# Optimization experiments

Hardware: AMD Instinct MI355X
Metric: run time of the kernel (lower is better)

## Reference

```python
import jax, jax.numpy as jnp
import numpy as np

D = 1024

def setup_inputs() -> dict:
    key = jax.random.key(0)
    ks = jax.random.split(key, 7)
    s = 1.0 / np.sqrt(D)
    return {
        "x": jax.random.normal(ks[0], (4, 2048, D), dtype=jnp.float32),
        "Wq": jax.random.uniform(ks[1], (D, D), jnp.float32, -s, s),
        "bq": jax.random.uniform(ks[2], (D,), jnp.float32, -s, s),
        "Wk": jax.random.uniform(ks[3], (D, D), jnp.float32, -s, s),
        "bk": jax.random.uniform(ks[4], (D,), jnp.float32, -s, s),
        "Wv": jax.random.uniform(ks[5], (D, D), jnp.float32, -s, s),
        "bv": jax.random.uniform(ks[6], (D,), jnp.float32, -s, s),
    }

def reference(x, Wq, bq, Wk, bk, Wv, bv):
    # x: [b, s, d]; Linear layers: y = x @ W^T + b (torch convention)
    q = jnp.einsum('bsd,ed->bse', x, Wq) + bq
    k = jnp.einsum('bsd,ed->bse', x, Wk) + bk
    v = jnp.einsum('bsd,ed->bse', x, Wv) + bv
    # NOTE: original module does NOT scale by 1/sqrt(d)
    scores = jnp.einsum('bqd,bkd->bqk', q, k)  # [b, s, s]
    attn = jax.nn.softmax(scores, axis=-1)
    return jnp.einsum('bqk,bkd->bqd', attn, v)
```

## Files before the change

kernel.cpp:

```cpp
#include <hip/hip_runtime.h>

typedef _Float16 half8 __attribute__((ext_vector_type(8)));
typedef float floatx4 __attribute__((ext_vector_type(4)));

__device__ __forceinline__ void gld_lds16(const void* g, void* l) {
  __builtin_amdgcn_global_load_lds(
      (const __attribute__((address_space(1))) void*)g,
      (__attribute__((address_space(3))) void*)l, 16, 0, 0);
}

#define SB() __builtin_amdgcn_sched_barrier(0)
#define LGKM(n) asm volatile("s_waitcnt lgkmcnt(" #n ")" ::: "memory")
#define VMC0() asm volatile("s_waitcnt vmcnt(0)" ::: "memory")
#define BAR() __builtin_amdgcn_s_barrier()
#define PRIO1() __builtin_amdgcn_s_setprio(1)
#define PRIO0() __builtin_amdgcn_s_setprio(0)

template <int MODE>
__global__ __launch_bounds__(512, 2) void gemmr(
    const _Float16* __restrict__ Ag, const _Float16* __restrict__ Bg,
    void* __restrict__ Cg, const float* __restrict__ bcat) {
  constexpr int TN   = MODE == 0 ? 192 : (MODE == 1 ? 256 : 128);
  constexpr int KS   = MODE == 0 ? 1024 : (MODE == 1 ? 3072 : 2048);
  constexpr int NK   = MODE == 2 ? 32 : 16;
  constexpr int NWG  = MODE == 0 ? 512 : 256;
  constexpr int WN   = MODE == 1 ? 4 : 2;
  constexpr int NMF  = MODE == 1 ? 8 : 4;
  constexpr int NNF  = TN / 16 / WN;
  constexpr int ASL  = 16384;
  constexpr int BSL  = TN * 64;
  constexpr int NSB  = TN / 64;
  constexpr int CSTR = MODE == 0 ? 3072 : (MODE == 1 ? 2048 : 1024);

  int g = (int)blockIdx.x;
  g = (g & 7) * (NWG / 8) + (g >> 3);

  int row0, col0;
  const _Float16 *Ap, *Bp;
  _Float16* C16 = nullptr;
  float* C32 = nullptr;
  if constexpr (MODE == 0) {
    const int tm = g >> 4, tn = g & 15;
    row0 = tm * 256; col0 = tn * 192;
    Ap = Ag + (size_t)row0 * 1024;
    Bp = Bg + (size_t)col0 * 1024;
    C16 = (_Float16*)Cg;
  } else if constexpr (MODE == 1) {
    const int z = g >> 6, r = g & 63, tm = r >> 3, tn = r & 7;
    row0 = tm * 256; col0 = tn * 256;
    Ap = Ag + (size_t)z * 6291456 + (size_t)row0 * 3072;
    Bp = Ag + (size_t)z * 6291456 + (size_t)col0 * 3072 + 1024;
    C16 = (_Float16*)Cg + (size_t)z * 4194304;
  } else {
    const int z = g >> 6, r = g & 63, tm = r >> 3, tn = r & 7;
    row0 = tm * 256; col0 = tn * 128;
    Ap = Ag + (size_t)z * 4194304 + (size_t)row0 * 2048;
    Bp = Bg + (size_t)z * 2097152 + (size_t)col0 * 2048;
    C32 = (float*)Cg + (size_t)z * 2097152;
  }

  __shared__ _Float16 lds[2 * ASL + 2 * BSL];
  const int tid = threadIdx.x, lane = tid & 63, wid = tid >> 6;
  const int wm = MODE == 1 ? (wid >> 2) : (wid >> 1);
  const int wn = MODE == 1 ? (wid & 3) : (wid & 1);
  const int wrow = wm * (NMF * 16);
  const int wcol = wn * (NNF * 16);
  const int fr = lane & 15, u = lane >> 4, w7 = lane & 7;
  const int k0e = ((u ^ w7) << 3), k1e = (((4 + u) ^ w7) << 3);
  const int srow = tid >> 3;
  const int sgl = (((tid & 7) ^ (srow & 7)) << 3);

  floatx4 acc[NMF][NNF] = {};
  half8 aF[NMF * 2], bF[NNF * 2];

  auto stage1 = [&](const _Float16* Gp, int rowoff, int kt, int dst) {
    gld_lds16(Gp + (size_t)(rowoff + srow) * KS + kt + sgl, &lds[dst + tid * 8]);
  };
  auto stageT = [&](int kt, int p) {
#pragma unroll
    for (int c = 0; c < 4; ++c) stage1(Ap, c * 64, kt, p * ASL + c * 4096);
#pragma unroll
    for (int c = 0; c < NSB; ++c)
      stage1(Bp, c * 64, kt, 2 * ASL + p * BSL + c * 4096);
  };
  auto ldA4 = [&](int p, int mf0) {
#pragma unroll
    for (int mf = 0; mf < 4; ++mf) {
      const int ro = p * ASL + (wrow + (mf0 + mf) * 16 + fr) * 64;
      aF[(mf0 + mf) * 2 + 0] = *(const half8*)&lds[ro + k0e];
      aF[(mf0 + mf) * 2 + 1] = *(const half8*)&lds[ro + k1e];
    }
  };
  auto ldB2 = [&](int p, int nf0) {
#pragma unroll
    for (int nf = 0; nf < 2; ++nf) {
      const int ro = 2 * ASL + p * BSL + (wcol + (nf0 + nf) * 16 + fr) * 64;
      bF[(nf0 + nf) * 2 + 0] = *(const half8*)&lds[ro + k0e];
      bF[(nf0 + nf) * 2 + 1] = *(const half8*)&lds[ro + k1e];
    }
  };
  auto burst = [&](int mf0, int nf0) {
#pragma unroll
    for (int mf = 0; mf < 4; ++mf)
#pragma unroll
      for (int nf = 0; nf < 2; ++nf)
#pragma unroll
        for (int kk = 0; kk < 2; ++kk)
          acc[mf0 + mf][nf0 + nf] = __builtin_amdgcn_mfma_f32_16x16x32_f16(
              aF[(mf0 + mf) * 2 + kk], bF[(nf0 + nf) * 2 + kk],
              acc[mf0 + mf][nf0 + nf], 0, 0, 0);
  };

  stageT(0, 0);
  VMC0();
  BAR();

#pragma unroll 1
  for (int t = 0; t < NK; ++t) {
    const int p = t & 1;
    if (t + 1 < NK) stageT(t * 64 + 64, p ^ 1);
    SB();
    if constexpr (MODE == 1) {
      ldA4(p, 0); SB(); ldB2(p, 0); SB(); ldB2(p, 2); SB(); ldA4(p, 4); SB();
      LGKM(12); SB(); PRIO1(); burst(0, 0); PRIO0(); SB();
      LGKM(8);  SB(); PRIO1(); burst(0, 2); PRIO0(); SB();
      LGKM(0);  SB(); PRIO1(); burst(4, 0); burst(4, 2); PRIO0(); SB();
    } else if constexpr (MODE == 0) {
      ldA4(p, 0); SB(); ldB2(p, 0); SB(); ldB2(p, 2); SB(); ldB2(p, 4); SB();
      LGKM(8); SB(); PRIO1(); burst(0, 0); PRIO0(); SB();
      LGKM(4); SB(); PRIO1(); burst(0, 2); PRIO0(); SB();
      LGKM(0); SB(); PRIO1(); burst(0, 4); PRIO0(); SB();
    } else {
      ldA4(p, 0); SB(); ldB2(p, 0); SB(); ldB2(p, 2); SB();
      LGKM(4); SB(); PRIO1(); burst(0, 0); PRIO0(); SB();
      LGKM(0); SB(); PRIO1(); burst(0, 2); PRIO0(); SB();
    }
    if (t + 1 < NK) VMC0();
    BAR();
  }

  const int r0 = row0 + wrow + u * 4;
  const int c0 = col0 + wcol + fr;
#pragma unroll
  for (int mf = 0; mf < NMF; ++mf)
#pragma unroll
    for (int nf = 0; nf < NNF; ++nf) {
      const int col = c0 + nf * 16;
      float badd = 0.f;
      if constexpr (MODE == 0) badd = bcat[col];
#pragma unroll
      for (int j = 0; j < 4; ++j) {
        const int row = r0 + mf * 16 + j;
        if constexpr (MODE == 2)
          C32[(size_t)row * CSTR + col] = acc[mf][nf][j];
        else
          C16[(size_t)row * CSTR + col] = (_Float16)(acc[mf][nf][j] + badd);
      }
    }
}

__global__ void cvt_f32_f16(const float* __restrict__ in, _Float16* __restrict__ out, int n8) {
  int i = blockIdx.x * blockDim.x + threadIdx.x;
  const int stride = gridDim.x * blockDim.x;
  for (; i < n8; i += stride) {
    const float4* p = (const float4*)(in + (size_t)i * 8);
    float4 a = p[0], b = p[1];
    half8 h;
    h[0] = (_Float16)a.x; h[1] = (_Float16)a.y; h[2] = (_Float16)a.z; h[3] = (_Float16)a.w;
    h[4] = (_Float16)b.x; h[5] = (_Float16)b.y; h[6] = (_Float16)b.z; h[7] = (_Float16)b.w;
    *(half8*)(out + (size_t)i * 8) = h;
  }
}

__global__ void cvt3_w(const float* __restrict__ wq, const float* __restrict__ wk,
                       const float* __restrict__ wv, _Float16* __restrict__ out) {
  const float* in = blockIdx.y == 0 ? wq : (blockIdx.y == 1 ? wk : wv);
  _Float16* o = out + (size_t)blockIdx.y * 1048576;
  const int i = blockIdx.x * blockDim.x + threadIdx.x;
  const float4* p = (const float4*)(in + (size_t)i * 8);
  float4 a = p[0], b = p[1];
  half8 h;
  h[0] = (_Float16)a.x; h[1] = (_Float16)a.y; h[2] = (_Float16)a.z; h[3] = (_Float16)a.w;
  h[4] = (_Float16)b.x; h[5] = (_Float16)b.y; h[6] = (_Float16)b.z; h[7] = (_Float16)b.w;
  *(half8*)(o + (size_t)i * 8) = h;
}

__global__ void bias_cat(const float* __restrict__ a, const float* __restrict__ b,
                         const float* __restrict__ c, float* __restrict__ o) {
  const int i = blockIdx.x * 256 + threadIdx.x;
  const float* s = i < 1024 ? a : (i < 2048 ? b : c);
  o[i] = s[i & 1023];
}

__global__ __launch_bounds__(256) void transpose_v(const _Float16* __restrict__ QKV,
                                                   _Float16* __restrict__ Vt) {
  __shared__ _Float16 t[32][36];
  const int b = blockIdx.z;
  const int e0 = blockIdx.x * 32;
  const int s0 = blockIdx.y * 32;
  const int tid = threadIdx.x;
  const int r = tid >> 3;
  const int c4 = (tid & 7) * 4;
  const _Float16* src = QKV + (size_t)(b * 2048 + s0 + r) * 3072 + 2048 + e0 + c4;
#pragma unroll
  for (int j = 0; j < 4; ++j) t[r][c4 + j] = src[j];
  __syncthreads();
  _Float16* dst = Vt + ((size_t)b * 1024 + e0 + r) * 2048 + s0 + c4;
#pragma unroll
  for (int j = 0; j < 4; ++j) dst[j] = t[c4 + j][r];
}

__global__ __launch_bounds__(256) void softmax_rows_f16(_Float16* __restrict__ S) {
  __shared__ float red[4];
  _Float16* s = S + (size_t)blockIdx.x * 2048;
  const int tid = threadIdx.x;
  float v[8];
  {
    half8 h = *(const half8*)(s + tid * 8);
#pragma unroll
    for (int j = 0; j < 8; ++j) v[j] = (float)h[j];
  }
  float m = v[0];
#pragma unroll
  for (int j = 1; j < 8; ++j) m = fmaxf(m, v[j]);
#pragma unroll
  for (int off = 32; off > 0; off >>= 1) m = fmaxf(m, __shfl_xor(m, off));
  if ((tid & 63) == 0) red[tid >> 6] = m;
  __syncthreads();
  m = fmaxf(fmaxf(red[0], red[1]), fmaxf(red[2], red[3]));
  float sum = 0.f;
#pragma unroll
  for (int j = 0; j < 8; ++j) { v[j] = __expf(v[j] - m); sum += v[j]; }
#pragma unroll
  for (int off = 32; off > 0; off >>= 1) sum += __shfl_xor(sum, off);
  __syncthreads();
  if ((tid & 63) == 0) red[tid >> 6] = sum;
  __syncthreads();
  sum = red[0] + red[1] + red[2] + red[3];
  const float inv = 1.0f / sum;
  half8 h;
#pragma unroll
  for (int j = 0; j < 8; ++j) h[j] = (_Float16)(v[j] * inv);
  *(half8*)(s + tid * 8) = h;
}

extern "C" void kernel_launch(void* const* d_in, const int* in_sizes, int n_in,
                              void* d_out, int out_size, void* d_ws, size_t ws_size,
                              hipStream_t stream) {
  (void)in_sizes; (void)n_in; (void)out_size;
  const float* x  = (const float*)d_in[0];
  const float* Wq = (const float*)d_in[1];
  const float* bq = (const float*)d_in[2];
  const float* Wk = (const float*)d_in[3];
  const float* bk = (const float*)d_in[4];
  const float* Wv = (const float*)d_in[5];
  const float* bv = (const float*)d_in[6];
  float* out = (float*)d_out;

  char* ws = (char*)d_ws;
  size_t off = 0;
  auto alloc = [&](size_t bytes) {
    char* p = ws + off;
    off += (bytes + 255) & ~255ull;
    return p;
  };
  _Float16* x16  = (_Float16*)alloc(8192ull * 1024 * 2);
  _Float16* W16  = (_Float16*)alloc(3072ull * 1024 * 2);
  _Float16* QKV  = (_Float16*)alloc(8192ull * 3072 * 2);
  _Float16* Vt   = (_Float16*)alloc(4096ull * 1024 * 4);
  _Float16* Sc   = (_Float16*)alloc(4ull * 2048 * 2048 * 2);
  float*    bcat = (float*)alloc(3072 * 4);
  if (off > ws_size) return;

  cvt_f32_f16<<<2048, 256, 0, stream>>>(x, x16, 8192 * 1024 / 8);
  cvt3_w<<<dim3(512, 3), 256, 0, stream>>>(Wq, Wk, Wv, W16);
  bias_cat<<<12, 256, 0, stream>>>(bq, bk, bv, bcat);

  gemmr<0><<<512, 512, 0, stream>>>(x16, W16, QKV, bcat);
  transpose_v<<<dim3(32, 64, 4), 256, 0, stream>>>(QKV, Vt);

  gemmr<1><<<256, 512, 0, stream>>>(QKV, QKV, Sc, nullptr);
  softmax_rows_f16<<<8192, 256, 0, stream>>>(Sc);
  gemmr<2><<<256, 512, 0, stream>>>(Sc, Vt, out, nullptr);
}
```

Before: 163.0 us.

## Use uniform 128x128 GEMM tiles with 256 threads and fuse prep kernels

Replaces the large per-mode GEMM tiles (256x192, 256x256, 256x128 with 512 threads) with a single 128x128 tile using 4 waves, which raises the workgroup count for all three GEMMs. The three small conversion/bias kernels are merged into one prep launch to cut launch overhead. Smaller tiles lower per-tile arithmetic intensity and add global/LDS traffic, but they fill the CUs better and use less LDS, so more workgroups can be resident.

After: 158.8 us. 2.5% less time.

```diff
diff --git a/kernel.cpp b/kernel.cpp
--- a/kernel.cpp
+++ b/kernel.cpp
@@ -17,19 +17,12 @@
 #define PRIO0() __builtin_amdgcn_s_setprio(0)
 
 template <int MODE>
-__global__ __launch_bounds__(512, 2) void gemmr(
+__global__ __launch_bounds__(256, 2) void gemmd(
     const _Float16* __restrict__ Ag, const _Float16* __restrict__ Bg,
     void* __restrict__ Cg, const float* __restrict__ bcat) {
-  constexpr int TN   = MODE == 0 ? 192 : (MODE == 1 ? 256 : 128);
   constexpr int KS   = MODE == 0 ? 1024 : (MODE == 1 ? 3072 : 2048);
   constexpr int NK   = MODE == 2 ? 32 : 16;
-  constexpr int NWG  = MODE == 0 ? 512 : 256;
-  constexpr int WN   = MODE == 1 ? 4 : 2;
-  constexpr int NMF  = MODE == 1 ? 8 : 4;
-  constexpr int NNF  = TN / 16 / WN;
-  constexpr int ASL  = 16384;
-  constexpr int BSL  = TN * 64;
-  constexpr int NSB  = TN / 64;
+  constexpr int NWG  = MODE == 0 ? 1536 : (MODE == 1 ? 1024 : 512);
   constexpr int CSTR = MODE == 0 ? 3072 : (MODE == 1 ? 2048 : 1024);
 
   int g = (int)blockIdx.x;
@@ -40,75 +33,71 @@
   _Float16* C16 = nullptr;
   float* C32 = nullptr;
   if constexpr (MODE == 0) {
-    const int tm = g >> 4, tn = g & 15;
-    row0 = tm * 256; col0 = tn * 192;
+    const int tm = g / 24, tn = g % 24;
+    row0 = tm * 128; col0 = tn * 128;
     Ap = Ag + (size_t)row0 * 1024;
     Bp = Bg + (size_t)col0 * 1024;
     C16 = (_Float16*)Cg;
   } else if constexpr (MODE == 1) {
-    const int z = g >> 6, r = g & 63, tm = r >> 3, tn = r & 7;
-    row0 = tm * 256; col0 = tn * 256;
+    const int z = g >> 8, r = g & 255, tm = r >> 4, tn = r & 15;
+    row0 = tm * 128; col0 = tn * 128;
     Ap = Ag + (size_t)z * 6291456 + (size_t)row0 * 3072;
     Bp = Ag + (size_t)z * 6291456 + (size_t)col0 * 3072 + 1024;
     C16 = (_Float16*)Cg + (size_t)z * 4194304;
   } else {
-    const int z = g >> 6, r = g & 63, tm = r >> 3, tn = r & 7;
-    row0 = tm * 256; col0 = tn * 128;
+    const int z = g >> 7, r = g & 127, tm = r >> 3, tn = r & 7;
+    row0 = tm * 128; col0 = tn * 128;
     Ap = Ag + (size_t)z * 4194304 + (size_t)row0 * 2048;
     Bp = Bg + (size_t)z * 2097152 + (size_t)col0 * 2048;
     C32 = (float*)Cg + (size_t)z * 2097152;
   }
 
-  __shared__ _Float16 lds[2 * ASL + 2 * BSL];
+  __shared__ _Float16 lds[32768];
   const int tid = threadIdx.x, lane = tid & 63, wid = tid >> 6;
-  const int wm = MODE == 1 ? (wid >> 2) : (wid >> 1);
-  const int wn = MODE == 1 ? (wid & 3) : (wid & 1);
-  const int wrow = wm * (NMF * 16);
-  const int wcol = wn * (NNF * 16);
+  const int wm = wid >> 1, wn = wid & 1;
+  const int wrow = wm * 64, wcol = wn * 64;
   const int fr = lane & 15, u = lane >> 4, w7 = lane & 7;
   const int k0e = ((u ^ w7) << 3), k1e = (((4 + u) ^ w7) << 3);
   const int srow = tid >> 3;
   const int sgl = (((tid & 7) ^ (srow & 7)) << 3);
 
-  floatx4 acc[NMF][NNF] = {};
-  half8 aF[NMF * 2], bF[NNF * 2];
+  floatx4 acc[4][4] = {};
+  half8 aF[8], bF[8];
 
   auto stage1 = [&](const _Float16* Gp, int rowoff, int kt, int dst) {
     gld_lds16(Gp + (size_t)(rowoff + srow) * KS + kt + sgl, &lds[dst + tid * 8]);
   };
   auto stageT = [&](int kt, int p) {
 #pragma unroll
-    for (int c = 0; c < 4; ++c) stage1(Ap, c * 64, kt, p * ASL + c * 4096);
-#pragma unroll
-    for (int c = 0; c < NSB; ++c)
-      stage1(Bp, c * 64, kt, 2 * ASL + p * BSL + c * 4096);
-  };
-  auto ldA4 = [&](int p, int mf0) {
+    for (int c = 0; c < 4; ++c) stage1(Ap, c * 32, kt, p * 8192 + c * 2048);
+#pragma unroll
+    for (int c = 0; c < 4; ++c) stage1(Bp, c * 32, kt, 16384 + p * 8192 + c * 2048);
+  };
+  auto ldA4 = [&](int p) {
 #pragma unroll
     for (int mf = 0; mf < 4; ++mf) {
-      const int ro = p * ASL + (wrow + (mf0 + mf) * 16 + fr) * 64;
-      aF[(mf0 + mf) * 2 + 0] = *(const half8*)&lds[ro + k0e];
-      aF[(mf0 + mf) * 2 + 1] = *(const half8*)&lds[ro + k1e];
+      const int ro = p * 8192 + (wrow + mf * 16 + fr) * 64;
+      aF[mf * 2 + 0] = *(const half8*)&lds[ro + k0e];
+      aF[mf * 2 + 1] = *(const half8*)&lds[ro + k1e];
     }
   };
   auto ldB2 = [&](int p, int nf0) {
 #pragma unroll
     for (int nf = 0; nf < 2; ++nf) {
-      const int ro = 2 * ASL + p * BSL + (wcol + (nf0 + nf) * 16 + fr) * 64;
+      const int ro = 16384 + p * 8192 + (wcol + (nf0 + nf) * 16 + fr) * 64;
       bF[(nf0 + nf) * 2 + 0] = *(const half8*)&lds[ro + k0e];
       bF[(nf0 + nf) * 2 + 1] = *(const half8*)&lds[ro + k1e];
     }
   };
-  auto burst = [&](int mf0, int nf0) {
+  auto burst = [&](int nf0) {
 #pragma unroll
     for (int mf = 0; mf < 4; ++mf)
 #pragma unroll
       for (int nf = 0; nf < 2; ++nf)
 #pragma unroll
         for (int kk = 0; kk < 2; ++kk)
-          acc[mf0 + mf][nf0 + nf] = __builtin_amdgcn_mfma_f32_16x16x32_f16(
-              aF[(mf0 + mf) * 2 + kk], bF[(nf0 + nf) * 2 + kk],
-              acc[mf0 + mf][nf0 + nf], 0, 0, 0);
+          acc[mf][nf0 + nf] = __builtin_amdgcn_mfma_f32_16x16x32_f16(
+              aF[mf * 2 + kk], bF[(nf0 + nf) * 2 + kk], acc[mf][nf0 + nf], 0, 0, 0);
   };
 
   stageT(0, 0);
@@ -120,21 +109,9 @@
     const int p = t & 1;
     if (t + 1 < NK) stageT(t * 64 + 64, p ^ 1);
     SB();
-    if constexpr (MODE == 1) {
-      ldA4(p, 0); SB(); ldB2(p, 0); SB(); ldB2(p, 2); SB(); ldA4(p, 4); SB();
-      LGKM(12); SB(); PRIO1(); burst(0, 0); PRIO0(); SB();
-      LGKM(8);  SB(); PRIO1(); burst(0, 2); PRIO0(); SB();
-      LGKM(0);  SB(); PRIO1(); burst(4, 0); burst(4, 2); PRIO0(); SB();
-    } else if constexpr (MODE == 0) {
-      ldA4(p, 0); SB(); ldB2(p, 0); SB(); ldB2(p, 2); SB(); ldB2(p, 4); SB();
-      LGKM(8); SB(); PRIO1(); burst(0, 0); PRIO0(); SB();
-      LGKM(4); SB(); PRIO1(); burst(0, 2); PRIO0(); SB();
-      LGKM(0); SB(); PRIO1(); burst(0, 4); PRIO0(); SB();
-    } else {
-      ldA4(p, 0); SB(); ldB2(p, 0); SB(); ldB2(p, 2); SB();
-      LGKM(4); SB(); PRIO1(); burst(0, 0); PRIO0(); SB();
-      LGKM(0); SB(); PRIO1(); burst(0, 2); PRIO0(); SB();
-    }
+    ldA4(p); SB(); ldB2(p, 0); SB(); ldB2(p, 2); SB();
+    LGKM(4); SB(); PRIO1(); burst(0); PRIO0(); SB();
+    LGKM(0); SB(); PRIO1(); burst(2); PRIO0(); SB();
     if (t + 1 < NK) VMC0();
     BAR();
   }
@@ -142,9 +119,9 @@
   const int r0 = row0 + wrow + u * 4;
   const int c0 = col0 + wcol + fr;
 #pragma unroll
-  for (int mf = 0; mf < NMF; ++mf)
-#pragma unroll
-    for (int nf = 0; nf < NNF; ++nf) {
+  for (int mf = 0; mf < 4; ++mf)
+#pragma unroll
+    for (int nf = 0; nf < 4; ++nf) {
       const int col = c0 + nf * 16;
       float badd = 0.f;
       if constexpr (MODE == 0) badd = bcat[col];
@@ -159,37 +136,38 @@
     }
 }
 
-__global__ void cvt_f32_f16(const float* __restrict__ in, _Float16* __restrict__ out, int n8) {
-  int i = blockIdx.x * blockDim.x + threadIdx.x;
-  const int stride = gridDim.x * blockDim.x;
-  for (; i < n8; i += stride) {
-    const float4* p = (const float4*)(in + (size_t)i * 8);
-    float4 a = p[0], b = p[1];
+__global__ __launch_bounds__(256) void prep(
+    const float* __restrict__ x, const float* __restrict__ wq,
+    const float* __restrict__ wk, const float* __restrict__ wv,
+    const float* __restrict__ bq, const float* __restrict__ bk,
+    const float* __restrict__ bv, _Float16* __restrict__ x16,
+    _Float16* __restrict__ W16, float* __restrict__ bcat) {
+  const int b = blockIdx.x, t = threadIdx.x;
+  auto cv8 = [](const float* src, _Float16* dst) {
+    const float4* p = (const float4*)src;
+    float4 a = p[0], bb = p[1];
     half8 h;
     h[0] = (_Float16)a.x; h[1] = (_Float16)a.y; h[2] = (_Float16)a.z; h[3] = (_Float16)a.w;
-    h[4] = (_Float16)b.x; h[5] = (_Float16)b.y; h[6] = (_Float16)b.z; h[7] = (_Float16)b.w;
-    *(half8*)(out + (size_t)i * 8) = h;
-  }
-}
-
-__global__ void cvt3_w(const float* __restrict__ wq, const float* __restrict__ wk,
-                       const float* __restrict__ wv, _Float16* __restrict__ out) {
-  const float* in = blockIdx.y == 0 ? wq : (blockIdx.y == 1 ? wk : wv);
-  _Float16* o = out + (size_t)blockIdx.y * 1048576;
-  const int i = blockIdx.x * blockDim.x + threadIdx.x;
-  const float4* p = (const float4*)(in + (size_t)i * 8);
-  float4 a = p[0], b = p[1];
-  half8 h;
-  h[0] = (_Float16)a.x; h[1] = (_Float16)a.y; h[2] = (_Float16)a.z; h[3] = (_Float16)a.w;
-  h[4] = (_Float16)b.x; h[5] = (_Float16)b.y; h[6] = (_Float16)b.z; h[7] = (_Float16)b.w;
-  *(half8*)(o + (size_t)i * 8) = h;
-}
-
-__global__ void bias_cat(const float* __restrict__ a, const float* __restrict__ b,
-                         const float* __restrict__ c, float* __restrict__ o) {
-  const int i = blockIdx.x * 256 + threadIdx.x;
-  const float* s = i < 1024 ? a : (i < 2048 ? b : c);
-  o[i] = s[i & 1023];
+    h[4] = (_Float16)bb.x; h[5] = (_Float16)bb.y; h[6] = (_Float16)bb.z; h[7] = (_Float16)bb.w;
+    *(half8*)dst = h;
+  };
+  if (b < 2048) {
+    const int i = b * 256 + t;
+#pragma unroll
+    for (int c = 0; c < 2; ++c) {
+      const size_t j = (size_t)(i + c * 524288) * 8;
+      cv8(x + j, x16 + j);
+    }
+  } else if (b < 3584) {
+    const int idx = (b - 2048) * 256 + t;
+    const int m = idx >> 17, j = idx & 131071;
+    const float* src = m == 0 ? wq : (m == 1 ? wk : wv);
+    cv8(src + (size_t)j * 8, W16 + (size_t)m * 1048576 + (size_t)j * 8);
+  } else {
+    const int i = (b - 3584) * 256 + t;
+    const float* s = i < 1024 ? bq : (i < 2048 ? bk : bv);
+    bcat[i] = s[i & 1023];
+  }
 }
 
 __global__ __launch_bounds__(256) void transpose_v(const _Float16* __restrict__ QKV,
@@ -272,14 +250,12 @@
   float*    bcat = (float*)alloc(3072 * 4);
   if (off > ws_size) return;
 
-  cvt_f32_f16<<<2048, 256, 0, stream>>>(x, x16, 8192 * 1024 / 8);
-  cvt3_w<<<dim3(512, 3), 256, 0, stream>>>(Wq, Wk, Wv, W16);
-  bias_cat<<<12, 256, 0, stream>>>(bq, bk, bv, bcat);
-
-  gemmr<0><<<512, 512, 0, stream>>>(x16, W16, QKV, bcat);
+  prep<<<3596, 256, 0, stream>>>(x, Wq, Wk, Wv, bq, bk, bv, x16, W16, bcat);
+
+  gemmd<0><<<1536, 256, 0, stream>>>(x16, W16, QKV, bcat);
   transpose_v<<<dim3(32, 64, 4), 256, 0, stream>>>(QKV, Vt);
 
-  gemmr<1><<<256, 512, 0, stream>>>(QKV, QKV, Sc, nullptr);
+  gemmd<1><<<1024, 256, 0, stream>>>(QKV, QKV, Sc, nullptr);
   softmax_rows_f16<<<8192, 256, 0, stream>>>(Sc);
-  gemmr<2><<<256, 512, 0, stream>>>(Sc, Vt, out, nullptr);
-}
+  gemmd<2><<<512, 256, 0, stream>>>(Sc, Vt, out, nullptr);
+}
```
